# Performance work log

Hardware: AMD Instinct MI355X
Metric: run time of the kernel (lower is better)

Reference implementation:

```python
import jax, jax.numpy as jnp
import numpy as np

DIM = 768
NUM_EXPERTS = 4
NUM_HEADS = 12
HEAD_DIM = DIM // NUM_HEADS
MLP_HID = 4 * DIM
FC1_OUT = MLP_HID + 3 * DIM   # 5376 (mlp hidden + qkv)
FC2_IN = MLP_HID + DIM        # 3840 (mlp hidden + attn out)
FC2_OUT = 2 * DIM             # 1536 (mlp out + attn proj out)
CAP_FACTOR = 0.5
LN_EPS = 1e-6


def setup_inputs() -> dict:
    key = jax.random.key(0)
    ks = jax.random.split(key, 4)
    B, N = 8, 1024
    return {
        "x": jax.random.normal(ks[0], (B, N, DIM), jnp.float32),
        "w_router": jax.random.normal(ks[1], (NUM_EXPERTS, DIM), jnp.float32) * 0.02,
        "gamma1": jnp.ones((DIM,), jnp.float32),
        "beta1": jnp.zeros((DIM,), jnp.float32),
        "w1": jax.random.normal(ks[2], (FC1_OUT, DIM), jnp.float32) * 0.02,
        "b1": jnp.zeros((FC1_OUT,), jnp.float32),
        "w2": jax.random.normal(ks[3], (FC2_OUT, FC2_IN), jnp.float32) * 0.02,
        "b2": jnp.zeros((FC2_OUT,), jnp.float32),
    }


def reference(x, w_router, gamma1, beta1, w1, b1, w2, b2):
    B, N, C = x.shape
    E = NUM_EXPERTS
    cap = int(CAP_FACTOR * N)
    # nested (MoNE) per-expert active dims: [96, 192, 384, 768] for E=4, C=768
    m = np.array([C // 2 ** (E - 1 - e) for e in range(E)])
    in_mask = (np.arange(C)[None, :] < m[:, None]).astype(np.float32)  # [E, C]
    in_mask = jnp.asarray(in_mask)
    out_mask = jnp.concatenate([in_mask, in_mask], axis=-1)  # [E, 2C] for fc2 chunks

    # ---- expert-choice router ----
    logits = jnp.einsum('bnc,ec->bne', x, w_router)          # [B, N, E]
    probs = jax.nn.softmax(logits, axis=-1)
    gate, idx = jax.lax.top_k(jnp.swapaxes(probs, 1, 2), cap)  # [B, E, cap]
    dispatch = jax.nn.one_hot(idx, N, dtype=x.dtype)           # [B, E, cap, N]
    combine = dispatch * gate[..., None]                       # [B, E, cap, N]

    # ---- norm1 ----
    mu = jnp.mean(x, -1, keepdims=True)
    var = jnp.var(x, -1, keepdims=True)
    y = (x - mu) * jax.lax.rsqrt(var + LN_EPS) * gamma1 + beta1

    # ---- experts_choose_masked_contract (fc1, nested input dims) ----
    xg = jnp.einsum('becn,bnd->becd', dispatch, y)             # gather [B,E,cap,C]
    xg = xg * in_mask[None, :, None, :]                        # nested expert slice
    h = jnp.einsum('becd,fd->becf', xg, w1) + b1               # [B,E,cap,FC1_OUT]
    h = jnp.einsum('becn,becf->bnf', dispatch, h)              # scatter [B,N,FC1_OUT]

    x_mlp, x_qkv = h[..., :MLP_HID], h[..., MLP_HID:]

    # ---- attention ----
    qkv = x_qkv.reshape(B, N, 3, NUM_HEADS, HEAD_DIM).transpose(2, 0, 3, 1, 4)
    q, k, v = qkv[0], qkv[1], qkv[2]                           # [B,H,N,hd]
    scale = HEAD_DIM ** -0.5
    attn = jax.nn.softmax(jnp.einsum('bhqd,bhkd->bhqk', q, k) * scale, axis=-1)
    x_attn = jnp.einsum('bhqk,bhkd->bhqd', attn, v)
    x_attn = x_attn.transpose(0, 2, 1, 3).reshape(B, N, C)

    # ---- mlp activation + concat ----
    x_mlp = jax.nn.gelu(x_mlp, approximate=False)
    y2 = jnp.concatenate([x_mlp, x_attn], axis=-1)             # [B,N,FC2_IN]

    # ---- experts_choose_masked_expand (fc2, nested output dims, combine-weighted) ----
    yg = jnp.einsum('becn,bnf->becf', dispatch, y2)            # gather [B,E,cap,FC2_IN]
    o = jnp.einsum('becf,of->beco', yg, w2) + b2               # [B,E,cap,FC2_OUT]
    o = o * out_mask[None, :, None, :]                         # nested expert output slice
    z = jnp.einsum('becn,beco->bno', combine, o)               # combine [B,N,FC2_OUT]

    x_mlp2, x_attn2 = z[..., :C], z[..., C:]
    return x + x_mlp2 + x_attn2
```

## Files before the change

kernel.cpp:

```cpp
#include <hip/hip_runtime.h>
#include <math.h>

typedef __bf16 bf16_t;
typedef __bf16 bf16x8 __attribute__((ext_vector_type(8)));
typedef __bf16 bf16x4 __attribute__((ext_vector_type(4)));
typedef float f32x4 __attribute__((ext_vector_type(4)));

#define DIM 768
#define NE 4
#define NH 12
#define HD 64
#define MLP_HID 3072
#define FC1_OUT 5376
#define FC2_IN 3840
#define CAP 512
#define LOG2E 1.44269504088896340736f

__device__ __forceinline__ void async_copy16(const void* g, void* l) {
  __builtin_amdgcn_global_load_lds((const __attribute__((address_space(1))) void*)g,
                                   (__attribute__((address_space(3))) void*)l, 16, 0, 0);
}

__device__ __forceinline__ float gelu_f(float v) {
  float v2 = v * v;
  float t = v * fmaf(-0.102944f, v2, -2.302208f);
  float e = exp2f(t);
  return v * __builtin_amdgcn_rcpf(1.0f + e);
}

__global__ __launch_bounds__(256) void cast_router_kernel(const float* __restrict__ w1,
                                                          const float* __restrict__ w2,
                                                          bf16_t* __restrict__ w1b,
                                                          bf16_t* __restrict__ w2b,
                                                          const float* __restrict__ x,
                                                          const float* __restrict__ wr,
                                                          float* __restrict__ probs) {
  if (blockIdx.x < 2048) {
    const int V1 = FC1_OUT * DIM / 4;
    const int V2 = 1536 * FC2_IN / 4;
    for (int i = blockIdx.x * 256 + threadIdx.x; i < V1 + V2; i += 2048 * 256) {
      if (i < V1) {
        float4 v = ((const float4*)w1)[i];
        bf16x4 pk = {(bf16_t)v.x, (bf16_t)v.y, (bf16_t)v.z, (bf16_t)v.w};
        *(bf16x4*)(w1b + i * 4) = pk;
      } else {
        int k = i - V1;
        float4 v = ((const float4*)w2)[k];
        bf16x4 pk = {(bf16_t)v.x, (bf16_t)v.y, (bf16_t)v.z, (bf16_t)v.w};
        *(bf16x4*)(w2b + k * 4) = pk;
      }
    }
    return;
  }
  int t = (blockIdx.x - 2048) * 4 + (threadIdx.x >> 6);
  int l = threadIdx.x & 63;
  const float* xr = x + (size_t)t * DIM;
  float a0 = 0.f, a1 = 0.f, a2 = 0.f, a3 = 0.f;
#pragma unroll
  for (int i = 0; i < 12; i++) {
    int d = l + i * 64;
    float xv = xr[d];
    a0 += xv * wr[d];
    a1 += xv * wr[DIM + d];
    a2 += xv * wr[2 * DIM + d];
    a3 += xv * wr[3 * DIM + d];
  }
#pragma unroll
  for (int off = 32; off > 0; off >>= 1) {
    a0 += __shfl_down(a0, off);
    a1 += __shfl_down(a1, off);
    a2 += __shfl_down(a2, off);
    a3 += __shfl_down(a3, off);
  }
  if (l == 0) {
    float m = fmaxf(fmaxf(a0, a1), fmaxf(a2, a3));
    float e0 = expf(a0 - m), e1 = expf(a1 - m), e2 = expf(a2 - m), e3 = expf(a3 - m);
    float inv = 1.0f / (e0 + e1 + e2 + e3);
    int b = t >> 10, n = t & 1023;
    probs[(b * NE + 0) * 1024 + n] = e0 * inv;
    probs[(b * NE + 1) * 1024 + n] = e1 * inv;
    probs[(b * NE + 2) * 1024 + n] = e2 * inv;
    probs[(b * NE + 3) * 1024 + n] = e3 * inv;
  }
}

__global__ __launch_bounds__(256) void rank_kernel(const float* __restrict__ probs,
                                                   float* __restrict__ gate_tok) {
  int be = blockIdx.y;
  __shared__ float p[1024];
  for (int i = threadIdx.x; i < 1024; i += 256) p[i] = probs[be * 1024 + i];
  __syncthreads();
  int n = blockIdx.x * 256 + threadIdx.x;
  float pn = p[n];
  int rank = 0;
  for (int j = 0; j < 1024; j++) {
    float pj = p[j];
    rank += (pj > pn) || (pj == pn && j < n);
  }
  int b = be >> 2, e = be & 3;
  gate_tok[(size_t)((b << 10) + n) * 4 + e] = (rank < CAP) ? pn : 0.0f;
}

__global__ __launch_bounds__(256) void ln_kernel(const float* __restrict__ x,
                                                 const float* __restrict__ gamma,
                                                 const float* __restrict__ beta,
                                                 const float* __restrict__ gate_tok,
                                                 bf16_t* __restrict__ ytil,
                                                 float* __restrict__ cntf,
                                                 float* __restrict__ g4) {
  int t = blockIdx.x * 4 + (threadIdx.x >> 6);
  int l = threadIdx.x & 63;
  float4 gg = ((const float4*)gate_tok)[t];
  float s0 = (gg.x > 0.f) ? 1.f : 0.f;
  float s1 = (gg.y > 0.f) ? 1.f : 0.f;
  float s2 = (gg.z > 0.f) ? 1.f : 0.f;
  float s3 = (gg.w > 0.f) ? 1.f : 0.f;
  float c3 = s3, c2 = c3 + s2, c1 = c2 + s1, c0 = c1 + s0;
  if (l == 0) {
    cntf[t] = c0;
    float4 G;
    G.x = gg.x + gg.y + gg.z + gg.w;
    G.y = gg.y + gg.z + gg.w;
    G.z = gg.z + gg.w;
    G.w = gg.w;
    ((float4*)g4)[t] = G;
  }
  const float* xr = x + (size_t)t * DIM + l * 12;
  float4 v4[3];
#pragma unroll
  for (int j = 0; j < 3; j++) v4[j] = *(const float4*)(xr + j * 4);
  float s = 0.f, sq = 0.f;
#pragma unroll
  for (int j = 0; j < 3; j++) {
    s += v4[j].x + v4[j].y + v4[j].z + v4[j].w;
    sq += v4[j].x * v4[j].x + v4[j].y * v4[j].y + v4[j].z * v4[j].z + v4[j].w * v4[j].w;
  }
#pragma unroll
  for (int off = 1; off < 64; off <<= 1) {
    s += __shfl_xor(s, off);
    sq += __shfl_xor(sq, off);
  }
  float mean = s * (1.0f / DIM);
  float var = sq * (1.0f / DIM) - mean * mean;
  float rs = rsqrtf(var + 1e-6f);
  int d0 = l * 12;
  float cf = (d0 < 96) ? c0 : (d0 < 192) ? c1 : (d0 < 384) ? c2 : c3;
  bf16_t* yo = ytil + (size_t)t * DIM + d0;
#pragma unroll
  for (int j = 0; j < 3; j++) {
    float4 gv = *(const float4*)(gamma + d0 + j * 4);
    float4 bv = *(const float4*)(beta + d0 + j * 4);
    bf16x4 pk;
    pk[0] = (bf16_t)(((v4[j].x - mean) * rs * gv.x + bv.x) * cf);
    pk[1] = (bf16_t)(((v4[j].y - mean) * rs * gv.y + bv.y) * cf);
    pk[2] = (bf16_t)(((v4[j].z - mean) * rs * gv.z + bv.z) * cf);
    pk[3] = (bf16_t)(((v4[j].w - mean) * rs * gv.w + bv.w) * cf);
    *(bf16x4*)(yo + j * 4) = pk;
  }
}

__global__ __launch_bounds__(256, 4) void fc1_kernel(const bf16_t* __restrict__ ytil,
                                                     const bf16_t* __restrict__ w1b,
                                                     const float* __restrict__ b1,
                                                     const float* __restrict__ cntf,
                                                     bf16_t* __restrict__ y2b,
                                                     bf16_t* __restrict__ qb,
                                                     bf16_t* __restrict__ kb,
                                                     bf16_t* __restrict__ vtb) {
  const int bid = blockIdx.x;
  const int xcd = bid & 7, j = bid >> 3;
  const int mt = xcd * 8 + (j & 7);
  const int nt = j >> 3;
  const int tid = threadIdx.x;
  const int w = tid >> 6, l = tid & 63;
  const int lq = l >> 4, lr = l & 15;

  __shared__ __align__(16) bf16_t lA[128 * 64];
  __shared__ __align__(16) bf16_t lB[128 * 64];

  f32x4 acc[4][4] = {};
  const int mwave = (w & 1) * 64, nwave = (w >> 1) * 64;
  const int crow = l >> 3;
  const int cbg = (l & 7) ^ (crow & 7);

  for (int k0 = 0; k0 < DIM; k0 += 64) {
#pragma unroll
    for (int i = 0; i < 4; i++) {
      int c = w * 4 + i;
      int row = c * 8 + crow;
      async_copy16(ytil + (size_t)(mt * 128 + row) * DIM + k0 + cbg * 8, lA + c * 512);
      async_copy16(w1b + (size_t)(nt * 128 + row) * DIM + k0 + cbg * 8, lB + c * 512);
    }
    __syncthreads();
#pragma unroll
    for (int ks = 0; ks < 2; ks++) {
      const int cbA = ((ks * 4 + lq) ^ (lr & 7)) * 8;
      bf16x8 af[4], bfr[4];
#pragma unroll
      for (int mi = 0; mi < 4; mi++)
        af[mi] = *(const bf16x8*)(lA + (mwave + mi * 16 + lr) * 64 + cbA);
#pragma unroll
      for (int ni = 0; ni < 4; ni++)
        bfr[ni] = *(const bf16x8*)(lB + (nwave + ni * 16 + lr) * 64 + cbA);
#pragma unroll
      for (int mi = 0; mi < 4; mi++)
#pragma unroll
        for (int ni = 0; ni < 4; ni++)
          acc[mi][ni] = __builtin_amdgcn_mfma_f32_16x16x32_bf16(af[mi], bfr[ni], acc[mi][ni], 0, 0, 0);
    }
    __syncthreads();
  }

#pragma unroll
  for (int mi = 0; mi < 4; mi++) {
    int row0 = mt * 128 + mwave + mi * 16 + lq * 4;
    float cnt[4];
#pragma unroll
    for (int r = 0; r < 4; r++) cnt[r] = cntf[row0 + r];
#pragma unroll
    for (int ni = 0; ni < 4; ni++) {
      int col = nt * 128 + nwave + ni * 16 + lr;
      float bias = b1[col];
      if (col < MLP_HID) {
#pragma unroll
        for (int r = 0; r < 4; r++) {
          float v = acc[mi][ni][r] + cnt[r] * bias;
          y2b[(size_t)(row0 + r) * FC2_IN + col] = (bf16_t)gelu_f(v);
        }
      } else {
        int part = col - MLP_HID;
        int comp = (part >= 1536) ? 2 : (part >= 768) ? 1 : 0;
        int rem = part - comp * 768;
        int hh = rem >> 6, d = rem & 63;
        int b = row0 >> 10, n0 = row0 & 1023;
        size_t base = (size_t)(b * NH + hh);
        if (comp == 2) {
          bf16x4 pk;
#pragma unroll
          for (int r = 0; r < 4; r++)
            pk[r] = (bf16_t)(acc[mi][ni][r] + cnt[r] * bias);
          *(bf16x4*)(vtb + (base * HD + d) * 1024 + n0) = pk;
        } else {
#pragma unroll
          for (int r = 0; r < 4; r++) {
            float v = acc[mi][ni][r] + cnt[r] * bias;
            if (comp == 0) qb[(base * 1024 + n0 + r) * HD + d] = (bf16_t)(v * (0.125f * LOG2E));
            else           kb[(base * 1024 + n0 + r) * HD + d] = (bf16_t)v;
          }
        }
      }
    }
  }
}

__global__ __launch_bounds__(256) void attn_kernel(const bf16_t* __restrict__ qb,
                                                   const bf16_t* __restrict__ kb,
                                                   const bf16_t* __restrict__ vtb,
                                                   bf16_t* __restrict__ y2b) {
  const int bid = blockIdx.x;
  const int xcd = bid & 7, j = bid >> 3;
  const int bh = xcd * 12 + (j >> 3);
  const int qt = j & 7;
  const int tid = threadIdx.x;
  const int w = tid >> 6, l = tid & 63, lq = l >> 4, lr = l & 15;

  __shared__ __align__(16) bf16_t lK[64 * 64];
  __shared__ __align__(16) bf16_t lV[64 * 64];
  __shared__ __align__(16) bf16_t lP[4][16 * 72];

  const bf16_t* qbase = qb + (size_t)bh * 1024 * HD;
  const bf16_t* kbase = kb + (size_t)bh * 1024 * HD;
  const bf16_t* vbase = vtb + (size_t)bh * HD * 1024;

  bf16x8 qf[2][2];
#pragma unroll
  for (int h = 0; h < 2; h++) {
    int qrow = qt * 128 + h * 64 + w * 16 + lr;
#pragma unroll
    for (int s = 0; s < 2; s++)
      qf[h][s] = *(const bf16x8*)(qbase + (size_t)qrow * HD + s * 32 + lq * 8);
  }

  f32x4 oacc[2][4] = {};
  float psum[2][4] = {};

  const int crow = l >> 3;
  const int cbg = (l & 7) ^ (crow & 7);

  for (int kt = 0; kt < 16; kt++) {
#pragma unroll
    for (int i = 0; i < 2; i++) {
      int c = w * 2 + i;
      int row = c * 8 + crow;
      async_copy16(kbase + (size_t)(kt * 64 + row) * HD + cbg * 8, lK + c * 512);
      async_copy16(vbase + (size_t)row * 1024 + kt * 64 + cbg * 8, lV + c * 512);
    }
    __syncthreads();

#pragma unroll
    for (int h = 0; h < 2; h++) {
      f32x4 sacc[4] = {};
#pragma unroll
      for (int s = 0; s < 2; s++) {
        const int cb = ((s * 4 + lq) ^ (lr & 7)) * 8;
#pragma unroll
        for (int kbq = 0; kbq < 4; kbq++) {
          bf16x8 kf = *(const bf16x8*)(lK + (kbq * 16 + lr) * 64 + cb);
          sacc[kbq] = __builtin_amdgcn_mfma_f32_16x16x32_bf16(qf[h][s], kf, sacc[kbq], 0, 0, 0);
        }
      }

#pragma unroll
      for (int kbq = 0; kbq < 4; kbq++)
#pragma unroll
        for (int r = 0; r < 4; r++) {
          float pv = exp2f(sacc[kbq][r]);
          psum[h][r] += pv;
          lP[w][(lq * 4 + r) * 72 + kbq * 16 + lr] = (bf16_t)pv;
        }

      bf16x8 pf[2];
#pragma unroll
      for (int s = 0; s < 2; s++)
        pf[s] = *(const bf16x8*)(&lP[w][lr * 72 + s * 32 + lq * 8]);

#pragma unroll
      for (int s = 0; s < 2; s++) {
        const int cb = ((s * 4 + lq) ^ (lr & 7)) * 8;
#pragma unroll
        for (int nb = 0; nb < 4; nb++) {
          bf16x8 vf = *(const bf16x8*)(lV + (nb * 16 + lr) * 64 + cb);
          oacc[h][nb] = __builtin_amdgcn_mfma_f32_16x16x32_bf16(pf[s], vf, oacc[h][nb], 0, 0, 0);
        }
      }
    }
    __syncthreads();
  }

  int b = bh / NH, hh = bh % NH;
#pragma unroll
  for (int h = 0; h < 2; h++) {
#pragma unroll
    for (int off = 1; off < 16; off <<= 1)
#pragma unroll
      for (int r = 0; r < 4; r++) psum[h][r] += __shfl_xor(psum[h][r], off);
    float rinv[4];
#pragma unroll
    for (int r = 0; r < 4; r++) rinv[r] = 1.0f / psum[h][r];
#pragma unroll
    for (int nb = 0; nb < 4; nb++)
#pragma unroll
      for (int r = 0; r < 4; r++) {
        float v = oacc[h][nb][r] * rinv[r];
        int tok = qt * 128 + h * 64 + w * 16 + lq * 4 + r;
        y2b[((size_t)(b * 1024 + tok)) * FC2_IN + MLP_HID + hh * HD + nb * 16 + lr] = (bf16_t)v;
      }
  }
}

__global__ __launch_bounds__(256, 4) void fc2_kernel(const bf16_t* __restrict__ y2b,
                                                     const bf16_t* __restrict__ w2b,
                                                     const float* __restrict__ b2,
                                                     const float* __restrict__ g4,
                                                     const float* __restrict__ x,
                                                     float* __restrict__ out) {
  const int bid = blockIdx.x;
  const int xcd = bid & 7, j = bid >> 3;
  const int mt = xcd * 8 + j / 12;
  const int ct = j % 12;
  const int tid = threadIdx.x;
  const int w = tid >> 6, l = tid & 63;
  const int lq = l >> 4, lr = l & 15;

  __shared__ __align__(16) bf16_t lA[128 * 64];
  __shared__ __align__(16) bf16_t lB[128 * 64];

  f32x4 acc[2][4][2] = {};
  const int mwave = (w & 1) * 64, nwave = (w >> 1) * 32;
  const int crow = l >> 3;
  const int cbg = (l & 7) ^ (crow & 7);

  for (int k0 = 0; k0 < FC2_IN; k0 += 64) {
#pragma unroll
    for (int i = 0; i < 4; i++) {
      int c = w * 4 + i;
      int row = c * 8 + crow;
      async_copy16(y2b + (size_t)(mt * 128 + row) * FC2_IN + k0 + cbg * 8, lA + c * 512);
      int grow = ((row >> 6) * 768) + ct * 64 + (row & 63);
      async_copy16(w2b + (size_t)grow * FC2_IN + k0 + cbg * 8, lB + c * 512);
    }
    __syncthreads();
#pragma unroll
    for (int ks = 0; ks < 2; ks++) {
      const int cbA = ((ks * 4 + lq) ^ (lr & 7)) * 8;
      bf16x8 af[4], bfr[2][2];
#pragma unroll
      for (int mi = 0; mi < 4; mi++)
        af[mi] = *(const bf16x8*)(lA + (mwave + mi * 16 + lr) * 64 + cbA);
#pragma unroll
      for (int h = 0; h < 2; h++)
#pragma unroll
        for (int ni = 0; ni < 2; ni++)
          bfr[h][ni] = *(const bf16x8*)(lB + (h * 64 + nwave + ni * 16 + lr) * 64 + cbA);
#pragma unroll
      for (int h = 0; h < 2; h++)
#pragma unroll
        for (int mi = 0; mi < 4; mi++)
#pragma unroll
          for (int ni = 0; ni < 2; ni++)
            acc[h][mi][ni] = __builtin_amdgcn_mfma_f32_16x16x32_bf16(af[mi], bfr[h][ni], acc[h][mi][ni], 0, 0, 0);
    }
    __syncthreads();
  }

#pragma unroll
  for (int mi = 0; mi < 4; mi++) {
    int row0 = mt * 128 + mwave + mi * 16 + lq * 4;
    float4 G[4];
#pragma unroll
    for (int r = 0; r < 4; r++) G[r] = ((const float4*)g4)[row0 + r];
#pragma unroll
    for (int ni = 0; ni < 2; ni++) {
      int col = ct * 64 + nwave + ni * 16 + lr;
      float b20 = b2[col], b21 = b2[768 + col];
#pragma unroll
      for (int r = 0; r < 4; r++) {
        float gw = (col < 96) ? G[r].x : (col < 192) ? G[r].y : (col < 384) ? G[r].z : G[r].w;
        float o = (acc[0][mi][ni][r] + b20) + (acc[1][mi][ni][r] + b21);
        size_t idx = (size_t)(row0 + r) * DIM + col;
        out[idx] = x[idx] + gw * o;
      }
    }
  }
}

extern "C" void kernel_launch(void* const* d_in, const int* in_sizes, int n_in,
                              void* d_out, int out_size, void* d_ws, size_t ws_size,
                              hipStream_t stream) {
  const float* x     = (const float*)d_in[0];
  const float* wr    = (const float*)d_in[1];
  const float* gamma = (const float*)d_in[2];
  const float* beta  = (const float*)d_in[3];
  const float* w1    = (const float*)d_in[4];
  const float* b1    = (const float*)d_in[5];
  const float* w2    = (const float*)d_in[6];
  const float* b2    = (const float*)d_in[7];
  float* out = (float*)d_out;

  char* ws = (char*)d_ws;
  float*  probs    = (float*)(ws + 0);
  float*  gate_tok = (float*)(ws + 131072);
  float*  cntf     = (float*)(ws + 262144);
  float*  g4       = (float*)(ws + 294912);
  bf16_t* w1b      = (bf16_t*)(ws + 425984);
  bf16_t* w2b      = (bf16_t*)(ws + 8683520);
  bf16_t* ytil     = (bf16_t*)(ws + 20480000);
  bf16_t* y2b      = (bf16_t*)(ws + 33062912);
  bf16_t* qb       = (bf16_t*)(ws + 95977472);
  bf16_t* kb       = (bf16_t*)(ws + 108560384);
  bf16_t* vtb      = (bf16_t*)(ws + 121143296);

  cast_router_kernel<<<4096, 256, 0, stream>>>(w1, w2, w1b, w2b, x, wr, probs);
  rank_kernel<<<dim3(4, 32), 256, 0, stream>>>(probs, gate_tok);
  ln_kernel<<<2048, 256, 0, stream>>>(x, gamma, beta, gate_tok, ytil, cntf, g4);
  fc1_kernel<<<2688, 256, 0, stream>>>(ytil, w1b, b1, cntf, y2b, qb, kb, vtb);
  attn_kernel<<<768, 256, 0, stream>>>(qb, kb, vtb, y2b);
  fc2_kernel<<<768, 256, 0, stream>>>(y2b, w2b, b2, g4, x, out);
}
```

Measured before the change: 380.0 us.

## Fuse top-k rank into layernorm kernel and halve fc2 column tile

The separate rank kernel and layernorm kernel are merged. Each layernorm block now computes expert-choice ranks for its 4 tokens across all 4 experts, with 16 lanes splitting each 1024-element comparison and a shuffle reduction. This removes a launch and the gate_tok round trip, but every block reloads the full 4x1024 probs row into LDS. Separately, fc2 switches to a 128x32 output tile with 1536 blocks and launch bounds raised to 6 for more parallelism and occupancy, at the cost of more redundant A-tile loads.

```diff
diff --git a/kernel.cpp b/kernel.cpp
--- a/kernel.cpp
+++ b/kernel.cpp
@@ -84,45 +84,56 @@
   }
 }
 
-__global__ __launch_bounds__(256) void rank_kernel(const float* __restrict__ probs,
-                                                   float* __restrict__ gate_tok) {
-  int be = blockIdx.y;
-  __shared__ float p[1024];
-  for (int i = threadIdx.x; i < 1024; i += 256) p[i] = probs[be * 1024 + i];
+__global__ __launch_bounds__(256) void rank_ln_kernel(const float* __restrict__ x,
+                                                      const float* __restrict__ gamma,
+                                                      const float* __restrict__ beta,
+                                                      const float* __restrict__ probs,
+                                                      bf16_t* __restrict__ ytil,
+                                                      float* __restrict__ cntf,
+                                                      float* __restrict__ g4) {
+  const int bid = blockIdx.x;
+  const int b = bid >> 8;
+  const int tid = threadIdx.x;
+  __shared__ float p[4][1024];
+  __shared__ float rankres[16];
+  for (int i = tid; i < 4096; i += 256)
+    p[i >> 10][i & 1023] = probs[((b * 4 + (i >> 10)) << 10) | (i & 1023)];
   __syncthreads();
-  int n = blockIdx.x * 256 + threadIdx.x;
-  float pn = p[n];
-  int rank = 0;
-  for (int j = 0; j < 1024; j++) {
-    float pj = p[j];
-    rank += (pj > pn) || (pj == pn && j < n);
-  }
-  int b = be >> 2, e = be & 3;
-  gate_tok[(size_t)((b << 10) + n) * 4 + e] = (rank < CAP) ? pn : 0.0f;
-}
-
-__global__ __launch_bounds__(256) void ln_kernel(const float* __restrict__ x,
-                                                 const float* __restrict__ gamma,
-                                                 const float* __restrict__ beta,
-                                                 const float* __restrict__ gate_tok,
-                                                 bf16_t* __restrict__ ytil,
-                                                 float* __restrict__ cntf,
-                                                 float* __restrict__ g4) {
-  int t = blockIdx.x * 4 + (threadIdx.x >> 6);
-  int l = threadIdx.x & 63;
-  float4 gg = ((const float4*)gate_tok)[t];
-  float s0 = (gg.x > 0.f) ? 1.f : 0.f;
-  float s1 = (gg.y > 0.f) ? 1.f : 0.f;
-  float s2 = (gg.z > 0.f) ? 1.f : 0.f;
-  float s3 = (gg.w > 0.f) ? 1.f : 0.f;
+  {
+    int pair = tid >> 4;
+    int tl = pair >> 2, e = pair & 3;
+    int lane16 = tid & 15;
+    int n = (bid & 255) * 4 + tl;
+    float pn = p[e][n];
+    int rank = 0;
+    int j0 = lane16 * 64;
+#pragma unroll 8
+    for (int jj = 0; jj < 64; jj++) {
+      float pj = p[e][j0 + jj];
+      rank += (pj > pn) || (pj == pn && (j0 + jj) < n);
+    }
+#pragma unroll
+    for (int off = 1; off < 16; off <<= 1) rank += __shfl_xor(rank, off);
+    if (lane16 == 0) rankres[pair] = (rank < CAP) ? pn : 0.0f;
+  }
+  __syncthreads();
+  const int tl = tid >> 6;
+  const int l = tid & 63;
+  const int t = bid * 4 + tl;
+  float gg0 = rankres[tl * 4 + 0], gg1 = rankres[tl * 4 + 1];
+  float gg2 = rankres[tl * 4 + 2], gg3 = rankres[tl * 4 + 3];
+  float s0 = (gg0 > 0.f) ? 1.f : 0.f;
+  float s1 = (gg1 > 0.f) ? 1.f : 0.f;
+  float s2 = (gg2 > 0.f) ? 1.f : 0.f;
+  float s3 = (gg3 > 0.f) ? 1.f : 0.f;
   float c3 = s3, c2 = c3 + s2, c1 = c2 + s1, c0 = c1 + s0;
   if (l == 0) {
     cntf[t] = c0;
     float4 G;
-    G.x = gg.x + gg.y + gg.z + gg.w;
-    G.y = gg.y + gg.z + gg.w;
-    G.z = gg.z + gg.w;
-    G.w = gg.w;
+    G.x = gg0 + gg1 + gg2 + gg3;
+    G.y = gg1 + gg2 + gg3;
+    G.z = gg2 + gg3;
+    G.w = gg3;
     ((float4*)g4)[t] = G;
   }
   const float* xr = x + (size_t)t * DIM + l * 12;
@@ -358,7 +369,7 @@
   }
 }
 
-__global__ __launch_bounds__(256, 4) void fc2_kernel(const bf16_t* __restrict__ y2b,
+__global__ __launch_bounds__(256, 6) void fc2_kernel(const bf16_t* __restrict__ y2b,
                                                      const bf16_t* __restrict__ w2b,
                                                      const float* __restrict__ b2,
                                                      const float* __restrict__ g4,
@@ -366,17 +377,17 @@
                                                      float* __restrict__ out) {
   const int bid = blockIdx.x;
   const int xcd = bid & 7, j = bid >> 3;
-  const int mt = xcd * 8 + j / 12;
-  const int ct = j % 12;
+  const int mt = xcd * 8 + j / 24;
+  const int ct = j % 24;
   const int tid = threadIdx.x;
   const int w = tid >> 6, l = tid & 63;
   const int lq = l >> 4, lr = l & 15;
 
   __shared__ __align__(16) bf16_t lA[128 * 64];
-  __shared__ __align__(16) bf16_t lB[128 * 64];
-
-  f32x4 acc[2][4][2] = {};
-  const int mwave = (w & 1) * 64, nwave = (w >> 1) * 32;
+  __shared__ __align__(16) bf16_t lB[64 * 64];
+
+  f32x4 acc[2][2][2] = {};
+  const int mwave = w * 32;
   const int crow = l >> 3;
   const int cbg = (l & 7) ^ (crow & 7);
 
@@ -386,26 +397,31 @@
       int c = w * 4 + i;
       int row = c * 8 + crow;
       async_copy16(y2b + (size_t)(mt * 128 + row) * FC2_IN + k0 + cbg * 8, lA + c * 512);
-      int grow = ((row >> 6) * 768) + ct * 64 + (row & 63);
+    }
+#pragma unroll
+    for (int i = 0; i < 2; i++) {
+      int c = w * 2 + i;
+      int row = c * 8 + crow;
+      int grow = (row >> 5) * 768 + ct * 32 + (row & 31);
       async_copy16(w2b + (size_t)grow * FC2_IN + k0 + cbg * 8, lB + c * 512);
     }
     __syncthreads();
 #pragma unroll
     for (int ks = 0; ks < 2; ks++) {
       const int cbA = ((ks * 4 + lq) ^ (lr & 7)) * 8;
-      bf16x8 af[4], bfr[2][2];
-#pragma unroll
-      for (int mi = 0; mi < 4; mi++)
+      bf16x8 af[2], bfr[2][2];
+#pragma unroll
+      for (int mi = 0; mi < 2; mi++)
         af[mi] = *(const bf16x8*)(lA + (mwave + mi * 16 + lr) * 64 + cbA);
 #pragma unroll
       for (int h = 0; h < 2; h++)
 #pragma unroll
         for (int ni = 0; ni < 2; ni++)
-          bfr[h][ni] = *(const bf16x8*)(lB + (h * 64 + nwave + ni * 16 + lr) * 64 + cbA);
+          bfr[h][ni] = *(const bf16x8*)(lB + (h * 32 + ni * 16 + lr) * 64 + cbA);
 #pragma unroll
       for (int h = 0; h < 2; h++)
 #pragma unroll
-        for (int mi = 0; mi < 4; mi++)
+        for (int mi = 0; mi < 2; mi++)
 #pragma unroll
           for (int ni = 0; ni < 2; ni++)
             acc[h][mi][ni] = __builtin_amdgcn_mfma_f32_16x16x32_bf16(af[mi], bfr[h][ni], acc[h][mi][ni], 0, 0, 0);
@@ -414,14 +430,14 @@
   }
 
 #pragma unroll
-  for (int mi = 0; mi < 4; mi++) {
+  for (int mi = 0; mi < 2; mi++) {
     int row0 = mt * 128 + mwave + mi * 16 + lq * 4;
     float4 G[4];
 #pragma unroll
     for (int r = 0; r < 4; r++) G[r] = ((const float4*)g4)[row0 + r];
 #pragma unroll
     for (int ni = 0; ni < 2; ni++) {
-      int col = ct * 64 + nwave + ni * 16 + lr;
+      int col = ct * 32 + ni * 16 + lr;
       float b20 = b2[col], b21 = b2[768 + col];
 #pragma unroll
       for (int r = 0; r < 4; r++) {
@@ -449,7 +465,6 @@
 
   char* ws = (char*)d_ws;
   float*  probs    = (float*)(ws + 0);
-  float*  gate_tok = (float*)(ws + 131072);
   float*  cntf     = (float*)(ws + 262144);
   float*  g4       = (float*)(ws + 294912);
   bf16_t* w1b      = (bf16_t*)(ws + 425984);
@@ -461,9 +476,8 @@
   bf16_t* vtb      = (bf16_t*)(ws + 121143296);
 
   cast_router_kernel<<<4096, 256, 0, stream>>>(w1, w2, w1b, w2b, x, wr, probs);
-  rank_kernel<<<dim3(4, 32), 256, 0, stream>>>(probs, gate_tok);
-  ln_kernel<<<2048, 256, 0, stream>>>(x, gamma, beta, gate_tok, ytil, cntf, g4);
+  rank_ln_kernel<<<2048, 256, 0, stream>>>(x, gamma, beta, probs, ytil, cntf, g4);
   fc1_kernel<<<2688, 256, 0, stream>>>(ytil, w1b, b1, cntf, y2b, qb, kb, vtb);
   attn_kernel<<<768, 256, 0, stream>>>(qb, kb, vtb, y2b);
-  fc2_kernel<<<768, 256, 0, stream>>>(y2b, w2b, b2, g4, x, out);
-}
+  fc2_kernel<<<1536, 256, 0, stream>>>(y2b, w2b, b2, g4, x, out);
+}
```

Measured after the change: 481.9 us. +26.8%, slower.
